# Kernel tuning notes

Hardware: AMD Instinct MI355X
Metric: run time of the kernel (lower is better)

The kernel has to match this reference:

```python
import jax, jax.numpy as jnp
import numpy as np

DT = 0.1
DEATH_THRESHOLD = 0.05


def setup_inputs() -> dict:
    key = jax.random.key(0)
    ks = jax.random.split(key, 12)
    B, S, DE, DM, DC, DEPTH = 1, 4096, 256, 64, 64, 4
    DIN = DE + DC
    w_scale = 0.02  # keeps pre-softmax scores in a sane range
    return {
        "e": jax.random.normal(ks[0], (B, S, DE), jnp.float32),
        "E": jax.random.uniform(ks[1], (B, S, 1), jnp.float32),
        "P": jax.random.uniform(ks[2], (B, S, 1), jnp.float32),
        "G": jax.random.normal(ks[3], (B, S, 1), jnp.float32),
        "m": jax.random.uniform(ks[4], (B, S, DM), jnp.float32),
        "c": jax.random.normal(ks[5], (B, S, DC), jnp.float32),
        "l": jax.random.uniform(ks[6], (B, S, 1), jnp.float32),
        "wq": jax.random.normal(ks[7], (DEPTH, DIN, DE), jnp.float32) * w_scale,
        "bq": jnp.zeros((DEPTH, DE), jnp.float32),
        "wk": jax.random.normal(ks[8], (DEPTH, DIN, DE), jnp.float32) * w_scale,
        "bk": jnp.zeros((DEPTH, DE), jnp.float32),
        "wv": jax.random.normal(ks[9], (DEPTH, DIN, DE), jnp.float32) * w_scale,
        "bv": jnp.zeros((DEPTH, DE), jnp.float32),
        "alpha": jnp.full((DEPTH,), 1.0, jnp.float32),
        "beta": jnp.full((DEPTH,), 0.5, jnp.float32),
        "gamma": jnp.full((DEPTH,), 0.2, jnp.float32),
        "basal": jnp.full((DEPTH,), 0.05, jnp.float32),
    }


def reference(e, E, P, G, m, c, l, wq, bq, wk, bk, wv, bv, alpha, beta, gamma, basal):
    depth = wq.shape[0]
    scale = 1.0 / np.sqrt(wq.shape[-1]).astype(np.float32)
    for i in range(depth):
        # --- OuterTrans: multiplicatively-masked self-attention ---
        x = jnp.concatenate([e, c], axis=-1)                 # [B,S,DE+DC]
        q = x @ wq[i] + bq[i]
        k = x @ wk[i] + bk[i]
        v = x @ wv[i] + bv[i]
        scores = jnp.einsum("bsd,btd->bst", q, k) * scale    # [B,S,S]
        membrane = jnp.einsum("bsd,btd->bst", m, m)          # [B,S,S]
        lifespan = jnp.einsum("bsd,btd->bst", l, l)          # [B,S,S]
        attn = jax.nn.softmax(scores * membrane * lifespan, axis=-1)
        h_tilde = jnp.einsum("bst,btd->bsd", attn, v)        # [B,S,DE]
        e = e + h_tilde
        # --- ThermodynamicODE (elementwise per-token update) ---
        S_in = jnp.sum(h_tilde * h_tilde, axis=-1, keepdims=True)  # ||h||^2 [B,S,1]
        PE = P * E
        P_new = jax.nn.relu(P + (alpha[i] * S_in - beta[i] * PE) * DT)
        E_new = jax.nn.relu(E + (basal[i] - gamma[i] * PE) * DT)
        m_target = jax.nn.sigmoid(E_new - P_new)             # [B,S,1] broadcast to m
        G = G + (0.1 * E_new - 0.5 * P_new) * DT
        l_decay = 0.01 + 0.5 * jax.nn.relu(P_new - 2.0)
        m = 0.9 * m + 0.1 * m_target
        l = jnp.clip(l - l_decay * DT, 0.0, 1.0)
        E, P = E_new, P_new
    # Dynamic pruning: jit-compatible variant -> zero-mask dead cells instead of
    # data-dependent slicing; also return alive_mask and num_died.
    alive = l > DEATH_THRESHOLD                              # [B,S,1] bool
    af = alive.astype(e.dtype)
    num_died = e.shape[1] - jnp.sum(alive.astype(jnp.int32))
    return (e * af, E * af, P * af, G * af, m * af, c * af, l * af,
            alive[0, :, 0], num_died)
```

## Files before the change

### kernel.cpp

```cpp
#include <hip/hip_runtime.h>
#include <hip/hip_bf16.h>
#include <math.h>

#define SS 4096
#define DE 256
#define DM 64
#define DC 64
#define DIN 320
#define DEPTH 4
#define DT_C 0.1f
#define NSPLIT 12
#define BK 32
#define EXP_SHIFT 8.0f

typedef float f32x4_t __attribute__((ext_vector_type(4)));
typedef __bf16 bf16x8_t __attribute__((ext_vector_type(8)));

#define MFMA_BF16(A, B, C) __builtin_amdgcn_mfma_f32_16x16x32_bf16((A), (B), (C), 0, 0, 0)

#define OFF_E     (SS*DE)
#define OFF_P     (OFF_E + SS)
#define OFF_G     (OFF_P + SS)
#define OFF_M     (OFF_G + SS)
#define OFF_C     (OFF_M + SS*DM)
#define OFF_L     (OFF_C + SS*DM)
#define OFF_ALIVE (OFF_L + SS)
#define OFF_DIED  (OFF_ALIVE + SS)

#define WS_EWS   0
#define WS_MWS   (WS_EWS  + SS*DE)
#define WS_EE    (WS_MWS  + SS*DM)
#define WS_PP    (WS_EE   + SS)
#define WS_GG    (WS_PP   + SS)
#define WS_LL    (WS_GG   + SS)
#define WS_PL    (WS_LL   + SS)
#define WS_POB   (WS_PL   + NSPLIT*SS)
#define WS_XB    (WS_POB  + NSPLIT*SS*DE/2)
#define WS_QB    (WS_XB   + SS*DIN/2)
#define WS_KB    (WS_QB   + SS*DE/2)
#define WS_VTB   (WS_KB   + SS*DE/2)
#define WS_MB    (WS_VTB  + SS*DE/2)
#define WS_WT    (WS_MB   + SS*DM/2)
#define WS_SEM   (WS_WT   + 3*DEPTH*DE*DIN/2)

#define KT_STR 264
#define VT_STR 40
#define PJ_STR 72

__global__ __launch_bounds__(256) void transpose_w_kernel(
    const float* __restrict__ wq, const float* __restrict__ wk, const float* __restrict__ wv,
    __hip_bfloat16* __restrict__ wt)
{
    const int zd = blockIdx.z;
    const int z = zd >> 2;
    const float* src = (z == 0 ? wq : (z == 1 ? wk : wv)) + (size_t)(zd & 3) * DIN * DE;
    __shared__ float t[32][33];
    const int k0 = blockIdx.x * 32;
    const int n0 = blockIdx.y * 32;
    const int tr = threadIdx.x >> 5;
    const int tc = threadIdx.x & 31;
    #pragma unroll
    for (int p = 0; p < 4; ++p)
        t[p*8 + tr][tc] = src[(size_t)(k0 + p*8 + tr) * DE + n0 + tc];
    __syncthreads();
    #pragma unroll
    for (int p = 0; p < 4; ++p) {
        int n = n0 + p*8 + tr;
        int k = k0 + tc;
        wt[((size_t)zd * DE + n) * DIN + k] = __float2bfloat16(t[tc][p*8 + tr]);
    }
}

__global__ __launch_bounds__(256) void init_kernel(
    const float* __restrict__ e_in, const float* __restrict__ c_in,
    const float* __restrict__ E_in, const float* __restrict__ P_in,
    const float* __restrict__ G_in, const float* __restrict__ l_in,
    const float* __restrict__ m_in,
    float* __restrict__ e_ws, __hip_bfloat16* __restrict__ xb,
    float* __restrict__ E_ws, float* __restrict__ P_ws, float* __restrict__ G_ws,
    float* __restrict__ l_ws, float* __restrict__ m_ws, __hip_bfloat16* __restrict__ mb,
    int* __restrict__ counters)
{
    const int row = blockIdx.x;
    const int tid = threadIdx.x;
    const float v = e_in[(size_t)row * DE + tid];
    e_ws[(size_t)row * DE + tid] = v;
    xb[(size_t)row * DIN + tid] = __float2bfloat16(v);
    if (tid < DC) {
        xb[(size_t)row * DIN + DE + tid] = __float2bfloat16(c_in[(size_t)row * DC + tid]);
        const float mv = m_in[(size_t)row * DM + tid];
        m_ws[(size_t)row * DM + tid] = mv;
        mb[(size_t)row * DM + tid] = __float2bfloat16(mv);
    }
    if (tid == 0) {
        E_ws[row] = E_in[row];
        P_ws[row] = P_in[row];
        G_ws[row] = G_in[row];
        l_ws[row] = l_in[row];
    }
    if (row == 0 && tid < 2) counters[tid] = 0;
}

__global__ __launch_bounds__(256, 4) void proj_gemm_kernel(
    const __hip_bfloat16* __restrict__ xb, const __hip_bfloat16* __restrict__ wt,
    const float* __restrict__ bq, const float* __restrict__ bk, const float* __restrict__ bv,
    __hip_bfloat16* __restrict__ qb, __hip_bfloat16* __restrict__ kb, __hip_bfloat16* __restrict__ vtb,
    int layer)
{
    __shared__ __align__(16) __hip_bfloat16 at[64 * PJ_STR];
    __shared__ __align__(16) __hip_bfloat16 bt[64 * PJ_STR];
    __shared__ __align__(16) __hip_bfloat16 tt[64 * PJ_STR];

    const int mt = blockIdx.x;
    const int nt4 = blockIdx.y;
    const int row0 = mt * 64;
    const int z = nt4 >> 2;
    const int coln0 = (nt4 & 3) * 64;
    const __hip_bfloat16* wrow = wt + ((size_t)(z * DEPTH + layer) * DE + coln0) * DIN;

    const int tid = threadIdx.x;
    const int w = tid >> 6, lane = tid & 63;
    const int ml = lane & 15, quad = lane >> 4;
    const int s_r = tid >> 2, s_g = tid & 3;

    f32x4_t acc[4];
    #pragma unroll
    for (int nt = 0; nt < 4; ++nt) acc[nt] = (f32x4_t){0.f, 0.f, 0.f, 0.f};

    for (int k0 = 0; k0 < DIN; k0 += 64) {
        __syncthreads();
        {
            const __hip_bfloat16* src = &xb[(size_t)(row0 + s_r) * DIN + k0 + s_g * 16];
            *(float4*)&at[s_r * PJ_STR + s_g * 16]     = *(const float4*)src;
            *(float4*)&at[s_r * PJ_STR + s_g * 16 + 8] = *(const float4*)(src + 8);
        }
        {
            const __hip_bfloat16* src = &wrow[(size_t)s_r * DIN + k0 + s_g * 16];
            *(float4*)&bt[s_r * PJ_STR + s_g * 16]     = *(const float4*)src;
            *(float4*)&bt[s_r * PJ_STR + s_g * 16 + 8] = *(const float4*)(src + 8);
        }
        __syncthreads();
        #pragma unroll
        for (int kk = 0; kk < 2; ++kk) {
            const bf16x8_t a = *(const bf16x8_t*)&at[(w * 16 + ml) * PJ_STR + kk * 32 + quad * 8];
            #pragma unroll
            for (int nt = 0; nt < 4; ++nt) {
                const bf16x8_t b = *(const bf16x8_t*)&bt[(nt * 16 + ml) * PJ_STR + kk * 32 + quad * 8];
                acc[nt] = MFMA_BF16(a, b, acc[nt]);
            }
        }
    }

    const float* bias = (z == 0 ? bq : (z == 1 ? bk : bv)) + (size_t)layer * DE;
    if (z < 2) {
        __hip_bfloat16* O = (z == 0 ? qb : kb);
        #pragma unroll
        for (int nt = 0; nt < 4; ++nt) {
            const int col = coln0 + nt * 16 + ml;
            const float b = bias[col];
            #pragma unroll
            for (int r = 0; r < 4; ++r)
                O[(size_t)(row0 + w * 16 + quad * 4 + r) * DE + col] = __float2bfloat16(acc[nt][r] + b);
        }
    } else {
        #pragma unroll
        for (int nt = 0; nt < 4; ++nt) {
            const int n = nt * 16 + ml;
            const float b = bias[coln0 + n];
            #pragma unroll
            for (int r = 0; r < 4; ++r)
                tt[n * PJ_STR + w * 16 + quad * 4 + r] = __float2bfloat16(acc[nt][r] + b);
        }
        __syncthreads();
        const int c = tid >> 2, seg = tid & 3;
        __hip_bfloat16* dst = &vtb[(size_t)(coln0 + c) * SS + row0 + seg * 16];
        *(float4*)dst       = *(const float4*)&tt[c * PJ_STR + seg * 16];
        *(float4*)(dst + 8) = *(const float4*)&tt[c * PJ_STR + seg * 16 + 8];
    }
}

__global__ __launch_bounds__(256, 3) void attn_mfma_kernel(
    const __hip_bfloat16* __restrict__ qb, const __hip_bfloat16* __restrict__ kb,
    const __hip_bfloat16* __restrict__ vtb, const __hip_bfloat16* __restrict__ mb,
    const float* __restrict__ l_ws,
    __hip_bfloat16* __restrict__ part_ob, float* __restrict__ part_l)
{
    __shared__ __align__(16) __hip_bfloat16 kt[32 * KT_STR];
    __shared__ __align__(16) __hip_bfloat16 vt[256 * VT_STR];

    const int id = blockIdx.x;
    const int split = id >> 6;
    const int rid = id & 63;
    const int qblk = (rid & 7) * 8 + (rid >> 3);

    const int tid = threadIdx.x;
    const int w = tid >> 6, lane = tid & 63;
    const int n = lane & 15, quad = lane >> 4;
    const int row0 = qblk * 64 + w * 16;

    bf16x8_t qa[8];
    #pragma unroll
    for (int kk = 0; kk < 8; ++kk)
        qa[kk] = *(const bf16x8_t*)&qb[(size_t)(row0 + n) * DE + kk * 32 + quad * 8];
    bf16x8_t ma[2];
    #pragma unroll
    for (int kk = 0; kk < 2; ++kk)
        ma[kk] = *(const bf16x8_t*)&mb[(size_t)(row0 + n) * DM + kk * 32 + quad * 8];
    const float lqs = l_ws[row0 + n] * 0.0625f;

    f32x4_t oacc[16];
    #pragma unroll
    for (int ct = 0; ct < 16; ++ct) oacc[ct] = (f32x4_t){0.f, 0.f, 0.f, 0.f};
    float plsum = 0.f;
    const f32x4_t zf4 = (f32x4_t){0.f, 0.f, 0.f, 0.f};

    const int k_row = tid >> 5, k_g = tid & 31;
    const int v_col = tid >> 2, v_seg = tid & 3;
    const int v_base = (v_seg & 1) * 16 + (v_seg >> 1) * 4;

    const int it_begin = (split * 128) / NSPLIT;
    const int it_end   = ((split + 1) * 128) / NSPLIT;

    for (int it = it_begin; it < it_end; ++it) {
        const int t0 = it * BK;
        __syncthreads();
        #pragma unroll
        for (int p = 0; p < 4; ++p) {
            const int row = k_row + p * 8;
            *(float4*)&kt[row * KT_STR + k_g * 8] = *(const float4*)&kb[(size_t)(t0 + row) * DE + k_g * 8];
        }
        #pragma unroll
        for (int p = 0; p < 4; ++p) {
            const int col = v_col + p * 64;
            const float4 f = *(const float4*)&vtb[(size_t)col * SS + t0 + v_seg * 8];
            *(float2*)&vt[col * VT_STR + v_base]     = make_float2(f.x, f.y);
            *(float2*)&vt[col * VT_STR + v_base + 8] = make_float2(f.z, f.w);
        }
        __syncthreads();

        const bf16x8_t mf00 = *(const bf16x8_t*)&mb[(size_t)(t0 + n) * DM + quad * 8];
        const bf16x8_t mf01 = *(const bf16x8_t*)&mb[(size_t)(t0 + n) * DM + 32 + quad * 8];
        const bf16x8_t mf10 = *(const bf16x8_t*)&mb[(size_t)(t0 + n + 16) * DM + quad * 8];
        const bf16x8_t mf11 = *(const bf16x8_t*)&mb[(size_t)(t0 + n + 16) * DM + 32 + quad * 8];
        const float4 lk0 = *(const float4*)&l_ws[t0 + quad * 4];
        const float4 lk1 = *(const float4*)&l_ws[t0 + 16 + quad * 4];

        f32x4_t s0a = zf4, s0b = zf4, s1a = zf4, s1b = zf4;
        #pragma unroll
        for (int kk = 0; kk < 4; ++kk) {
            bf16x8_t k0 = *(const bf16x8_t*)&kt[n * KT_STR + kk * 32 + quad * 8];
            bf16x8_t k1 = *(const bf16x8_t*)&kt[(n + 16) * KT_STR + kk * 32 + quad * 8];
            s0a = MFMA_BF16(k0, qa[kk], s0a);
            s1a = MFMA_BF16(k1, qa[kk], s1a);
        }
        #pragma unroll
        for (int kk = 4; kk < 8; ++kk) {
            bf16x8_t k0 = *(const bf16x8_t*)&kt[n * KT_STR + kk * 32 + quad * 8];
            bf16x8_t k1 = *(const bf16x8_t*)&kt[(n + 16) * KT_STR + kk * 32 + quad * 8];
            s0b = MFMA_BF16(k0, qa[kk], s0b);
            s1b = MFMA_BF16(k1, qa[kk], s1b);
        }
        const f32x4_t st0 = s0a + s0b;
        const f32x4_t st1 = s1a + s1b;

        f32x4_t mm0 = MFMA_BF16(mf00, ma[0], zf4);
        mm0 = MFMA_BF16(mf01, ma[1], mm0);
        f32x4_t mm1 = MFMA_BF16(mf10, ma[0], zf4);
        mm1 = MFMA_BF16(mf11, ma[1], mm1);

        bf16x8_t pa;
        #pragma unroll
        for (int r = 0; r < 4; ++r) {
            const float x0 = st0[r] * lqs * lk0[r] * mm0[r];
            const float x1 = st1[r] * lqs * lk1[r] * mm1[r];
            const float p0 = __expf(x0 - EXP_SHIFT);
            const float p1 = __expf(x1 - EXP_SHIFT);
            plsum += p0 + p1;
            pa[r]     = (__bf16)p0;
            pa[4 + r] = (__bf16)p1;
        }

        #pragma unroll
        for (int ct = 0; ct < 16; ++ct) {
            bf16x8_t vb = *(const bf16x8_t*)&vt[(ct * 16 + n) * VT_STR + quad * 8];
            oacc[ct] = MFMA_BF16(pa, vb, oacc[ct]);
        }
    }

    plsum += __shfl_xor(plsum, 16);
    plsum += __shfl_xor(plsum, 32);
    if (lane < 16)
        part_l[split * SS + row0 + lane] = plsum;

    __hip_bfloat16* dst = part_ob + ((size_t)((split * (SS / 64) + qblk) * 4 + w)) * 4096;
    #pragma unroll
    for (int ct = 0; ct < 16; ++ct) {
        __hip_bfloat16 h4[4];
        #pragma unroll
        for (int r = 0; r < 4; ++r) h4[r] = __float2bfloat16(oacc[ct][r]);
        *(uint2*)&dst[(ct * 64 + lane) * 4] = *(uint2*)h4;
    }
}

__global__ __launch_bounds__(256) void combine_kernel(
    const __hip_bfloat16* __restrict__ part_ob, const float* __restrict__ part_l,
    float* __restrict__ e_ws, __hip_bfloat16* __restrict__ xb,
    float* __restrict__ E_ws, float* __restrict__ P_ws, float* __restrict__ G_ws,
    float* __restrict__ m_ws, __hip_bfloat16* __restrict__ mb, float* __restrict__ l_ws,
    const float* __restrict__ alpha, const float* __restrict__ beta,
    const float* __restrict__ gamma_, const float* __restrict__ basal, int layer)
{
    const int wc = threadIdx.x >> 6, lane = threadIdx.x & 63;
    const int row = blockIdx.x * 4 + wc;
    const int qblk = row >> 6, wa = (row >> 4) & 3, quada = (row >> 2) & 3, ra = row & 3;

    float L = 0.f;
    #pragma unroll
    for (int s = 0; s < NSPLIT; ++s) L += part_l[s * SS + row];
    const float invL = 1.0f / L;

    const int ct = lane >> 2;
    const int base_off = (ct * 64 + quada * 16 + (lane & 3) * 4) * 4;
    float o[4] = {0.f, 0.f, 0.f, 0.f};
    #pragma unroll
    for (int s = 0; s < NSPLIT; ++s) {
        const size_t region = ((size_t)((s * (SS / 64) + qblk) * 4 + wa)) * 4096;
        const ushort* pp = (const ushort*)(part_ob + region) + base_off;
        ushort vals[16];
        *(uint4*)&vals[0] = *(const uint4*)pp;
        *(uint4*)&vals[8] = *(const uint4*)(pp + 8);
        #pragma unroll
        for (int j = 0; j < 4; ++j)
            o[j] += __uint_as_float(((unsigned)vals[j * 4 + ra]) << 16);
    }
    float h0 = o[0] * invL, h1 = o[1] * invL, h2 = o[2] * invL, h3 = o[3] * invL;

    float4 ev = *(float4*)&e_ws[(size_t)row * DE + lane * 4];
    ev.x += h0; ev.y += h1; ev.z += h2; ev.w += h3;
    *(float4*)&e_ws[(size_t)row * DE + lane * 4] = ev;
    {
        __hip_bfloat16 x4[4] = {__float2bfloat16(ev.x), __float2bfloat16(ev.y),
                                __float2bfloat16(ev.z), __float2bfloat16(ev.w)};
        *(uint2*)&xb[(size_t)row * DIN + lane * 4] = *(uint2*)x4;
    }

    float ssq = h0*h0 + h1*h1 + h2*h2 + h3*h3;
    #pragma unroll
    for (int mask = 1; mask < 64; mask <<= 1) ssq += __shfl_xor(ssq, mask);

    const float a = alpha[layer], b = beta[layer], gm = gamma_[layer], bas = basal[layer];
    const float E = E_ws[row], P = P_ws[row];
    const float PE = P * E;
    const float Pn = fmaxf(0.f, P + (a * ssq - b * PE) * DT_C);
    const float En = fmaxf(0.f, E + (bas - gm * PE) * DT_C);
    const float mtg = 1.f / (1.f + __expf(-(En - Pn)));
    const size_t mi = (size_t)row * DM + lane;
    const float mv = 0.9f * m_ws[mi] + 0.1f * mtg;
    m_ws[mi] = mv;
    mb[mi] = __float2bfloat16(mv);
    if (lane == 0) {
        E_ws[row] = En;
        P_ws[row] = Pn;
        G_ws[row] = G_ws[row] + (0.1f * En - 0.5f * Pn) * DT_C;
        const float ldec = 0.01f + 0.5f * fmaxf(0.f, Pn - 2.0f);
        const float lv = l_ws[row] - ldec * DT_C;
        l_ws[row] = fminf(1.f, fmaxf(0.f, lv));
    }
}

__global__ __launch_bounds__(256) void finalizec_kernel(
    const __hip_bfloat16* __restrict__ part_ob, const float* __restrict__ part_l,
    const float* __restrict__ e_ws,
    const float* __restrict__ E_ws, const float* __restrict__ P_ws, const float* __restrict__ G_ws,
    const float* __restrict__ m_ws, const float* __restrict__ c_in, const float* __restrict__ l_ws,
    const float* __restrict__ alpha, const float* __restrict__ beta,
    const float* __restrict__ gamma_, const float* __restrict__ basal,
    float* __restrict__ out, int* __restrict__ counters)
{
    const int rb = blockIdx.x;
    const int tid = threadIdx.x;
    const int wc = tid >> 6, lane = tid & 63;

    const int lp = DEPTH - 1;
    const float a = alpha[lp], bb = beta[lp], gm = gamma_[lp], bas = basal[lp];

    __shared__ int s_alive[4];
    int alive_cnt = 0;

    #pragma unroll
    for (int rr = 0; rr < 4; ++rr) {
        const int row = rb * 16 + wc * 4 + rr;
        const int qb2 = row >> 6, wa = (row >> 4) & 3, quada = (row >> 2) & 3, ra = row & 3;
        float L = 0.f;
        #pragma unroll
        for (int s = 0; s < NSPLIT; ++s) L += part_l[s * SS + row];
        const float invL = 1.0f / L;
        const int ct = lane >> 2;
        const int base_off = (ct * 64 + quada * 16 + (lane & 3) * 4) * 4;
        float o[4] = {0.f, 0.f, 0.f, 0.f};
        #pragma unroll
        for (int s = 0; s < NSPLIT; ++s) {
            const size_t region = ((size_t)((s * (SS / 64) + qb2) * 4 + wa)) * 4096;
            const ushort* pp = (const ushort*)(part_ob + region) + base_off;
            ushort vals[16];
            *(uint4*)&vals[0] = *(const uint4*)pp;
            *(uint4*)&vals[8] = *(const uint4*)(pp + 8);
            #pragma unroll
            for (int j = 0; j < 4; ++j)
                o[j] += __uint_as_float(((unsigned)vals[j * 4 + ra]) << 16);
        }
        const float h0 = o[0] * invL, h1 = o[1] * invL, h2 = o[2] * invL, h3 = o[3] * invL;
        float4 ev = *(const float4*)&e_ws[(size_t)row * DE + lane * 4];
        ev.x += h0; ev.y += h1; ev.z += h2; ev.w += h3;

        float ssq = h0*h0 + h1*h1 + h2*h2 + h3*h3;
        #pragma unroll
        for (int mask = 1; mask < 64; mask <<= 1) ssq += __shfl_xor(ssq, mask);

        const float E = E_ws[row], P = P_ws[row];
        const float PE = P * E;
        const float Pn = fmaxf(0.f, P + (a * ssq - bb * PE) * DT_C);
        const float En = fmaxf(0.f, E + (bas - gm * PE) * DT_C);
        const float mtg = 1.f / (1.f + __expf(-(En - Pn)));
        const float mv = 0.9f * m_ws[(size_t)row * DM + lane] + 0.1f * mtg;
        const float Gn = G_ws[row] + (0.1f * En - 0.5f * Pn) * DT_C;
        const float ldec = 0.01f + 0.5f * fmaxf(0.f, Pn - 2.0f);
        const float lv = fminf(1.f, fmaxf(0.f, l_ws[row] - ldec * DT_C));
        const float af = (lv > 0.05f) ? 1.f : 0.f;

        float4 eo = make_float4(ev.x * af, ev.y * af, ev.z * af, ev.w * af);
        *(float4*)&out[(size_t)row * DE + lane * 4] = eo;
        out[OFF_M + (size_t)row * DM + lane] = mv * af;
        out[OFF_C + (size_t)row * DM + lane] = c_in[(size_t)row * DM + lane] * af;
        if (lane == 0) {
            out[OFF_E + row] = En * af;
            out[OFF_P + row] = Pn * af;
            out[OFF_G + row] = Gn * af;
            out[OFF_L + row] = lv * af;
            out[OFF_ALIVE + row] = af;
            alive_cnt += (af > 0.f) ? 1 : 0;
        }
    }

    if (lane == 0) s_alive[wc] = alive_cnt;
    __syncthreads();
    if (tid == 0) {
        const int blk_alive = s_alive[0] + s_alive[1] + s_alive[2] + s_alive[3];
        atomicAdd(&counters[0], blk_alive);
        __threadfence();
        const int old = atomicAdd(&counters[1], 1);
        if (old == 255) {
            __threadfence();
            const int tot = atomicAdd(&counters[0], 0);
            out[OFF_DIED] = (float)(SS - tot);
        }
    }
}

extern "C" void kernel_launch(void* const* d_in, const int* in_sizes, int n_in,
                              void* d_out, int out_size, void* d_ws, size_t ws_size,
                              hipStream_t stream) {
    const float* e_in = (const float*)d_in[0];
    const float* E_in = (const float*)d_in[1];
    const float* P_in = (const float*)d_in[2];
    const float* G_in = (const float*)d_in[3];
    const float* m_in = (const float*)d_in[4];
    const float* c_in = (const float*)d_in[5];
    const float* l_in = (const float*)d_in[6];
    const float* wq = (const float*)d_in[7];
    const float* bq = (const float*)d_in[8];
    const float* wk = (const float*)d_in[9];
    const float* bk = (const float*)d_in[10];
    const float* wv = (const float*)d_in[11];
    const float* bv = (const float*)d_in[12];
    const float* alpha = (const float*)d_in[13];
    const float* beta  = (const float*)d_in[14];
    const float* gamma_ = (const float*)d_in[15];
    const float* basal = (const float*)d_in[16];
    float* out = (float*)d_out;
    float* ws = (float*)d_ws;

    float* e_ws = ws + WS_EWS;
    float* m_ws = ws + WS_MWS;
    float* E_ws = ws + WS_EE;
    float* P_ws = ws + WS_PP;
    float* G_ws = ws + WS_GG;
    float* l_ws = ws + WS_LL;
    float* part_l = ws + WS_PL;
    __hip_bfloat16* part_ob = (__hip_bfloat16*)(ws + WS_POB);
    __hip_bfloat16* xb  = (__hip_bfloat16*)(ws + WS_XB);
    __hip_bfloat16* qb  = (__hip_bfloat16*)(ws + WS_QB);
    __hip_bfloat16* kb  = (__hip_bfloat16*)(ws + WS_KB);
    __hip_bfloat16* vtb = (__hip_bfloat16*)(ws + WS_VTB);
    __hip_bfloat16* mb  = (__hip_bfloat16*)(ws + WS_MB);
    __hip_bfloat16* wt  = (__hip_bfloat16*)(ws + WS_WT);
    int* counters = (int*)(ws + WS_SEM);

    transpose_w_kernel<<<dim3(DIN/32, DE/32, 12), 256, 0, stream>>>(wq, wk, wv, wt);
    init_kernel<<<dim3(SS), 256, 0, stream>>>(
        e_in, c_in, E_in, P_in, G_in, l_in, m_in,
        e_ws, xb, E_ws, P_ws, G_ws, l_ws, m_ws, mb, counters);

    for (int layer = 0; layer < DEPTH; ++layer) {
        proj_gemm_kernel<<<dim3(SS/64, 12), 256, 0, stream>>>(
            xb, wt, bq, bk, bv, qb, kb, vtb, layer);
        attn_mfma_kernel<<<dim3((SS/64) * NSPLIT), 256, 0, stream>>>(
            qb, kb, vtb, mb, l_ws, part_ob, part_l);
        if (layer < DEPTH - 1)
            combine_kernel<<<dim3(SS/4), 256, 0, stream>>>(
                part_ob, part_l, e_ws, xb, E_ws, P_ws, G_ws, m_ws, mb, l_ws,
                alpha, beta, gamma_, basal, layer);
    }
    finalizec_kernel<<<dim3(SS/16), 256, 0, stream>>>(
        part_ob, part_l, e_ws, E_ws, P_ws, G_ws, m_ws, c_in, l_ws,
        alpha, beta, gamma_, basal, out, counters);
}
```

Baseline: 415.3 us.

## Fuse all layer stages into one persistent cooperative kernel with grid syncs

Replaces the sequence of transpose, init, projection, attention, combine and finalize launches with a single cooperative persistent kernel. Blocks loop over work items of each stage and use grid-wide barriers between stages. This removes per-launch overhead and tail gaps between the roughly fourteen kernels. The cost is grid.sync overhead, occupancy capped by the launch bounds and the shared-memory union, and load imbalance across fixed block counts. The old multi-kernel path stays as a fallback if the cooperative launch fails.

```diff
diff --git a/kernel.cpp b/kernel.cpp
--- a/kernel.cpp
+++ b/kernel.cpp
@@ -1,6 +1,9 @@
 #include <hip/hip_runtime.h>
+#include <hip/hip_cooperative_groups.h>
 #include <hip/hip_bf16.h>
 #include <math.h>
+
+namespace cg = cooperative_groups;
 
 #define SS 4096
 #define DE 256
@@ -12,6 +15,7 @@
 #define NSPLIT 12
 #define BK 32
 #define EXP_SHIFT 8.0f
+#define NBLK_MAX 768
 
 typedef float f32x4_t __attribute__((ext_vector_type(4)));
 typedef __bf16 bf16x8_t __attribute__((ext_vector_type(8)));
@@ -47,6 +51,397 @@
 #define VT_STR 40
 #define PJ_STR 72
 
+struct KParams {
+    const float *e_in, *c_in, *E_in, *P_in, *G_in, *l_in, *m_in;
+    const float *wq, *bq, *wk, *bk, *wv, *bv, *alpha, *beta, *gamma_, *basal;
+    float *e_ws, *m_ws, *E_ws, *P_ws, *G_ws, *l_ws, *part_l;
+    __hip_bfloat16 *part_ob, *xb, *qb, *kb, *vtb, *mb, *wt;
+    int* counters;
+    float* out;
+};
+
+__global__ __launch_bounds__(256, 3) void mega_kernel(KParams p)
+{
+    cg::grid_group grid = cg::this_grid();
+    __shared__ __align__(16) char smem[37376];
+    __shared__ int s_alive[4];
+    const int bid = blockIdx.x;
+    const int tid = threadIdx.x;
+    const int NB = gridDim.x;
+
+    {
+        float (*t)[33] = (float(*)[33])smem;
+        const int tr = tid >> 5, tc = tid & 31;
+        for (int s = bid; s < 960; s += NB) {
+            const int zd = s / 80;
+            const int rem = s % 80;
+            const int k0 = (rem >> 3) * 32;
+            const int n0 = (rem & 7) * 32;
+            const int z = zd >> 2;
+            const float* src = (z == 0 ? p.wq : (z == 1 ? p.wk : p.wv)) + (size_t)(zd & 3) * DIN * DE;
+            __syncthreads();
+            #pragma unroll
+            for (int q = 0; q < 4; ++q)
+                t[q*8 + tr][tc] = src[(size_t)(k0 + q*8 + tr) * DE + n0 + tc];
+            __syncthreads();
+            #pragma unroll
+            for (int q = 0; q < 4; ++q) {
+                const int n = n0 + q*8 + tr;
+                const int k = k0 + tc;
+                p.wt[((size_t)zd * DE + n) * DIN + k] = __float2bfloat16(t[tc][q*8 + tr]);
+            }
+        }
+        for (int row = bid; row < SS; row += NB) {
+            const float v = p.e_in[(size_t)row * DE + tid];
+            p.e_ws[(size_t)row * DE + tid] = v;
+            p.xb[(size_t)row * DIN + tid] = __float2bfloat16(v);
+            if (tid < DC) {
+                p.xb[(size_t)row * DIN + DE + tid] = __float2bfloat16(p.c_in[(size_t)row * DC + tid]);
+                const float mv = p.m_in[(size_t)row * DM + tid];
+                p.m_ws[(size_t)row * DM + tid] = mv;
+                p.mb[(size_t)row * DM + tid] = __float2bfloat16(mv);
+            }
+            if (tid == 0) {
+                p.E_ws[row] = p.E_in[row];
+                p.P_ws[row] = p.P_in[row];
+                p.G_ws[row] = p.G_in[row];
+                p.l_ws[row] = p.l_in[row];
+            }
+        }
+        if (bid == 0 && tid == 0) p.counters[0] = 0;
+    }
+    grid.sync();
+
+    for (int layer = 0; layer < DEPTH; ++layer) {
+        {
+            __hip_bfloat16* at  = (__hip_bfloat16*)smem;
+            __hip_bfloat16* btl = at + 64 * PJ_STR;
+            __hip_bfloat16* tt  = btl + 64 * PJ_STR;
+            const int w = tid >> 6, lane = tid & 63;
+            const int ml = lane & 15, quad = lane >> 4;
+            const int s_r = tid >> 2, s_g = tid & 3;
+
+            for (int s = bid; s < 768; s += NB) {
+                const int mt = s & 63, nt4 = s >> 6;
+                const int row0 = mt * 64;
+                const int z = nt4 >> 2;
+                const int coln0 = (nt4 & 3) * 64;
+                const __hip_bfloat16* wrow = p.wt + ((size_t)(z * DEPTH + layer) * DE + coln0) * DIN;
+
+                f32x4_t acc[4];
+                #pragma unroll
+                for (int nt = 0; nt < 4; ++nt) acc[nt] = (f32x4_t){0.f, 0.f, 0.f, 0.f};
+
+                for (int k0 = 0; k0 < DIN; k0 += 64) {
+                    __syncthreads();
+                    {
+                        const __hip_bfloat16* src = &p.xb[(size_t)(row0 + s_r) * DIN + k0 + s_g * 16];
+                        *(float4*)&at[s_r * PJ_STR + s_g * 16]     = *(const float4*)src;
+                        *(float4*)&at[s_r * PJ_STR + s_g * 16 + 8] = *(const float4*)(src + 8);
+                    }
+                    {
+                        const __hip_bfloat16* src = &wrow[(size_t)s_r * DIN + k0 + s_g * 16];
+                        *(float4*)&btl[s_r * PJ_STR + s_g * 16]     = *(const float4*)src;
+                        *(float4*)&btl[s_r * PJ_STR + s_g * 16 + 8] = *(const float4*)(src + 8);
+                    }
+                    __syncthreads();
+                    #pragma unroll
+                    for (int kk = 0; kk < 2; ++kk) {
+                        const bf16x8_t a = *(const bf16x8_t*)&at[(w * 16 + ml) * PJ_STR + kk * 32 + quad * 8];
+                        #pragma unroll
+                        for (int nt = 0; nt < 4; ++nt) {
+                            const bf16x8_t b = *(const bf16x8_t*)&btl[(nt * 16 + ml) * PJ_STR + kk * 32 + quad * 8];
+                            acc[nt] = MFMA_BF16(a, b, acc[nt]);
+                        }
+                    }
+                }
+
+                const float* bias = (z == 0 ? p.bq : (z == 1 ? p.bk : p.bv)) + (size_t)layer * DE;
+                if (z < 2) {
+                    __hip_bfloat16* O = (z == 0 ? p.qb : p.kb);
+                    #pragma unroll
+                    for (int nt = 0; nt < 4; ++nt) {
+                        const int col = coln0 + nt * 16 + ml;
+                        const float b = bias[col];
+                        #pragma unroll
+                        for (int r = 0; r < 4; ++r)
+                            O[(size_t)(row0 + w * 16 + quad * 4 + r) * DE + col] = __float2bfloat16(acc[nt][r] + b);
+                    }
+                } else {
+                    __syncthreads();
+                    #pragma unroll
+                    for (int nt = 0; nt < 4; ++nt) {
+                        const int n = nt * 16 + ml;
+                        const float b = bias[coln0 + n];
+                        #pragma unroll
+                        for (int r = 0; r < 4; ++r)
+                            tt[n * PJ_STR + w * 16 + quad * 4 + r] = __float2bfloat16(acc[nt][r] + b);
+                    }
+                    __syncthreads();
+                    const int c = tid >> 2, seg = tid & 3;
+                    __hip_bfloat16* dst = &p.vtb[(size_t)(coln0 + c) * SS + row0 + seg * 16];
+                    *(float4*)dst       = *(const float4*)&tt[c * PJ_STR + seg * 16];
+                    *(float4*)(dst + 8) = *(const float4*)&tt[c * PJ_STR + seg * 16 + 8];
+                }
+            }
+        }
+        grid.sync();
+
+        {
+            __hip_bfloat16* kt = (__hip_bfloat16*)smem;
+            __hip_bfloat16* vt = kt + 32 * KT_STR;
+            const int w = tid >> 6, lane = tid & 63;
+            const int n = lane & 15, quad = lane >> 4;
+            const int k_row = tid >> 5, k_g = tid & 31;
+            const int v_col = tid >> 2, v_seg = tid & 3;
+            const int v_base = (v_seg & 1) * 16 + (v_seg >> 1) * 4;
+            const f32x4_t zf4 = (f32x4_t){0.f, 0.f, 0.f, 0.f};
+
+            for (int s = bid; s < 768; s += NB) {
+                const int split = s >> 6;
+                const int rid = s & 63;
+                const int qblk = (rid & 7) * 8 + (rid >> 3);
+                const int row0 = qblk * 64 + w * 16;
+
+                bf16x8_t qa[8];
+                #pragma unroll
+                for (int kk = 0; kk < 8; ++kk)
+                    qa[kk] = *(const bf16x8_t*)&p.qb[(size_t)(row0 + n) * DE + kk * 32 + quad * 8];
+                bf16x8_t ma[2];
+                #pragma unroll
+                for (int kk = 0; kk < 2; ++kk)
+                    ma[kk] = *(const bf16x8_t*)&p.mb[(size_t)(row0 + n) * DM + kk * 32 + quad * 8];
+                const float lqs = p.l_ws[row0 + n] * 0.0625f;
+
+                f32x4_t oacc[16];
+                #pragma unroll
+                for (int ct = 0; ct < 16; ++ct) oacc[ct] = (f32x4_t){0.f, 0.f, 0.f, 0.f};
+                float plsum = 0.f;
+
+                const int it_begin = (split * 128) / NSPLIT;
+                const int it_end   = ((split + 1) * 128) / NSPLIT;
+
+                for (int it = it_begin; it < it_end; ++it) {
+                    const int t0 = it * BK;
+                    __syncthreads();
+                    #pragma unroll
+                    for (int q = 0; q < 4; ++q) {
+                        const int row = k_row + q * 8;
+                        *(float4*)&kt[row * KT_STR + k_g * 8] = *(const float4*)&p.kb[(size_t)(t0 + row) * DE + k_g * 8];
+                    }
+                    #pragma unroll
+                    for (int q = 0; q < 4; ++q) {
+                        const int col = v_col + q * 64;
+                        const float4 f = *(const float4*)&p.vtb[(size_t)col * SS + t0 + v_seg * 8];
+                        *(float2*)&vt[col * VT_STR + v_base]     = make_float2(f.x, f.y);
+                        *(float2*)&vt[col * VT_STR + v_base + 8] = make_float2(f.z, f.w);
+                    }
+                    __syncthreads();
+
+                    const bf16x8_t mf00 = *(const bf16x8_t*)&p.mb[(size_t)(t0 + n) * DM + quad * 8];
+                    const bf16x8_t mf01 = *(const bf16x8_t*)&p.mb[(size_t)(t0 + n) * DM + 32 + quad * 8];
+                    const bf16x8_t mf10 = *(const bf16x8_t*)&p.mb[(size_t)(t0 + n + 16) * DM + quad * 8];
+                    const bf16x8_t mf11 = *(const bf16x8_t*)&p.mb[(size_t)(t0 + n + 16) * DM + 32 + quad * 8];
+                    const float4 lk0 = *(const float4*)&p.l_ws[t0 + quad * 4];
+                    const float4 lk1 = *(const float4*)&p.l_ws[t0 + 16 + quad * 4];
+
+                    f32x4_t s0a = zf4, s0b = zf4, s1a = zf4, s1b = zf4;
+                    #pragma unroll
+                    for (int kk = 0; kk < 4; ++kk) {
+                        bf16x8_t k0 = *(const bf16x8_t*)&kt[n * KT_STR + kk * 32 + quad * 8];
+                        bf16x8_t k1 = *(const bf16x8_t*)&kt[(n + 16) * KT_STR + kk * 32 + quad * 8];
+                        s0a = MFMA_BF16(k0, qa[kk], s0a);
+                        s1a = MFMA_BF16(k1, qa[kk], s1a);
+                    }
+                    #pragma unroll
+                    for (int kk = 4; kk < 8; ++kk) {
+                        bf16x8_t k0 = *(const bf16x8_t*)&kt[n * KT_STR + kk * 32 + quad * 8];
+                        bf16x8_t k1 = *(const bf16x8_t*)&kt[(n + 16) * KT_STR + kk * 32 + quad * 8];
+                        s0b = MFMA_BF16(k0, qa[kk], s0b);
+                        s1b = MFMA_BF16(k1, qa[kk], s1b);
+                    }
+                    const f32x4_t st0 = s0a + s0b;
+                    const f32x4_t st1 = s1a + s1b;
+
+                    f32x4_t mm0 = MFMA_BF16(mf00, ma[0], zf4);
+                    mm0 = MFMA_BF16(mf01, ma[1], mm0);
+                    f32x4_t mm1 = MFMA_BF16(mf10, ma[0], zf4);
+                    mm1 = MFMA_BF16(mf11, ma[1], mm1);
+
+                    bf16x8_t pa;
+                    #pragma unroll
+                    for (int r = 0; r < 4; ++r) {
+                        const float x0 = st0[r] * lqs * lk0[r] * mm0[r];
+                        const float x1 = st1[r] * lqs * lk1[r] * mm1[r];
+                        const float p0 = __expf(x0 - EXP_SHIFT);
+                        const float p1 = __expf(x1 - EXP_SHIFT);
+                        plsum += p0 + p1;
+                        pa[r]     = (__bf16)p0;
+                        pa[4 + r] = (__bf16)p1;
+                    }
+
+                    #pragma unroll
+                    for (int ct = 0; ct < 16; ++ct) {
+                        bf16x8_t vb = *(const bf16x8_t*)&vt[(ct * 16 + n) * VT_STR + quad * 8];
+                        oacc[ct] = MFMA_BF16(pa, vb, oacc[ct]);
+                    }
+                }
+
+                plsum += __shfl_xor(plsum, 16);
+                plsum += __shfl_xor(plsum, 32);
+                if (lane < 16)
+                    p.part_l[split * SS + row0 + lane] = plsum;
+
+                __hip_bfloat16* dst = p.part_ob + ((size_t)((split * (SS / 64) + qblk) * 4 + w)) * 4096;
+                #pragma unroll
+                for (int ct = 0; ct < 16; ++ct) {
+                    __hip_bfloat16 h4[4];
+                    #pragma unroll
+                    for (int r = 0; r < 4; ++r) h4[r] = __float2bfloat16(oacc[ct][r]);
+                    *(uint2*)&dst[(ct * 64 + lane) * 4] = *(uint2*)h4;
+                }
+                __syncthreads();
+            }
+        }
+        grid.sync();
+
+        if (layer < DEPTH - 1) {
+            const int wc = tid >> 6, lane = tid & 63;
+            for (int grp = bid; grp < SS / 4; grp += NB) {
+                const int row = grp * 4 + wc;
+                const int qblk = row >> 6, wa = (row >> 4) & 3, quada = (row >> 2) & 3, ra = row & 3;
+
+                float L = 0.f;
+                #pragma unroll
+                for (int s = 0; s < NSPLIT; ++s) L += p.part_l[s * SS + row];
+                const float invL = 1.0f / L;
+
+                const int ct = lane >> 2;
+                const int base_off = (ct * 64 + quada * 16 + (lane & 3) * 4) * 4;
+                float o[4] = {0.f, 0.f, 0.f, 0.f};
+                #pragma unroll
+                for (int s = 0; s < NSPLIT; ++s) {
+                    const size_t region = ((size_t)((s * (SS / 64) + qblk) * 4 + wa)) * 4096;
+                    const ushort* pp = (const ushort*)(p.part_ob + region) + base_off;
+                    ushort vals[16];
+                    *(uint4*)&vals[0] = *(const uint4*)pp;
+                    *(uint4*)&vals[8] = *(const uint4*)(pp + 8);
+                    #pragma unroll
+                    for (int j = 0; j < 4; ++j)
+                        o[j] += __uint_as_float(((unsigned)vals[j * 4 + ra]) << 16);
+                }
+                const float h0 = o[0] * invL, h1 = o[1] * invL, h2 = o[2] * invL, h3 = o[3] * invL;
+
+                float4 ev = *(float4*)&p.e_ws[(size_t)row * DE + lane * 4];
+                ev.x += h0; ev.y += h1; ev.z += h2; ev.w += h3;
+                *(float4*)&p.e_ws[(size_t)row * DE + lane * 4] = ev;
+                {
+                    __hip_bfloat16 x4[4] = {__float2bfloat16(ev.x), __float2bfloat16(ev.y),
+                                            __float2bfloat16(ev.z), __float2bfloat16(ev.w)};
+                    *(uint2*)&p.xb[(size_t)row * DIN + lane * 4] = *(uint2*)x4;
+                }
+
+                float ssq = h0*h0 + h1*h1 + h2*h2 + h3*h3;
+                #pragma unroll
+                for (int mask = 1; mask < 64; mask <<= 1) ssq += __shfl_xor(ssq, mask);
+
+                const float a = p.alpha[layer], b = p.beta[layer], gm = p.gamma_[layer], bas = p.basal[layer];
+                const float E = p.E_ws[row], P = p.P_ws[row];
+                const float PE = P * E;
+                const float Pn = fmaxf(0.f, P + (a * ssq - b * PE) * DT_C);
+                const float En = fmaxf(0.f, E + (bas - gm * PE) * DT_C);
+                const float mtg = 1.f / (1.f + __expf(-(En - Pn)));
+                const size_t mi = (size_t)row * DM + lane;
+                const float mv = 0.9f * p.m_ws[mi] + 0.1f * mtg;
+                p.m_ws[mi] = mv;
+                p.mb[mi] = __float2bfloat16(mv);
+                if (lane == 0) {
+                    p.E_ws[row] = En;
+                    p.P_ws[row] = Pn;
+                    p.G_ws[row] = p.G_ws[row] + (0.1f * En - 0.5f * Pn) * DT_C;
+                    const float ldec = 0.01f + 0.5f * fmaxf(0.f, Pn - 2.0f);
+                    const float lv = p.l_ws[row] - ldec * DT_C;
+                    p.l_ws[row] = fminf(1.f, fmaxf(0.f, lv));
+                }
+            }
+            grid.sync();
+        }
+    }
+
+    {
+        const int wc = tid >> 6, lane = tid & 63;
+        const int lp = DEPTH - 1;
+        const float a = p.alpha[lp], bb = p.beta[lp], gm = p.gamma_[lp], bas = p.basal[lp];
+
+        for (int grp = bid; grp < SS / 16; grp += NB) {
+            int alive_cnt = 0;
+            #pragma unroll
+            for (int rr = 0; rr < 4; ++rr) {
+                const int row = grp * 16 + wc * 4 + rr;
+                const int qb2 = row >> 6, wa = (row >> 4) & 3, quada = (row >> 2) & 3, ra = row & 3;
+                float L = 0.f;
+                #pragma unroll
+                for (int s = 0; s < NSPLIT; ++s) L += p.part_l[s * SS + row];
+                const float invL = 1.0f / L;
+                const int ct = lane >> 2;
+                const int base_off = (ct * 64 + quada * 16 + (lane & 3) * 4) * 4;
+                float o[4] = {0.f, 0.f, 0.f, 0.f};
+                #pragma unroll
+                for (int s = 0; s < NSPLIT; ++s) {
+                    const size_t region = ((size_t)((s * (SS / 64) + qb2) * 4 + wa)) * 4096;
+                    const ushort* pp = (const ushort*)(p.part_ob + region) + base_off;
+                    ushort vals[16];
+                    *(uint4*)&vals[0] = *(const uint4*)pp;
+                    *(uint4*)&vals[8] = *(const uint4*)(pp + 8);
+                    #pragma unroll
+                    for (int j = 0; j < 4; ++j)
+                        o[j] += __uint_as_float(((unsigned)vals[j * 4 + ra]) << 16);
+                }
+                const float h0 = o[0] * invL, h1 = o[1] * invL, h2 = o[2] * invL, h3 = o[3] * invL;
+                float4 ev = *(const float4*)&p.e_ws[(size_t)row * DE + lane * 4];
+                ev.x += h0; ev.y += h1; ev.z += h2; ev.w += h3;
+
+                float ssq = h0*h0 + h1*h1 + h2*h2 + h3*h3;
+                #pragma unroll
+                for (int mask = 1; mask < 64; mask <<= 1) ssq += __shfl_xor(ssq, mask);
+
+                const float E = p.E_ws[row], P = p.P_ws[row];
+                const float PE = P * E;
+                const float Pn = fmaxf(0.f, P + (a * ssq - bb * PE) * DT_C);
+                const float En = fmaxf(0.f, E + (bas - gm * PE) * DT_C);
+                const float mtg = 1.f / (1.f + __expf(-(En - Pn)));
+                const float mv = 0.9f * p.m_ws[(size_t)row * DM + lane] + 0.1f * mtg;
+                const float Gn = p.G_ws[row] + (0.1f * En - 0.5f * Pn) * DT_C;
+                const float ldec = 0.01f + 0.5f * fmaxf(0.f, Pn - 2.0f);
+                const float lv = fminf(1.f, fmaxf(0.f, p.l_ws[row] - ldec * DT_C));
+                const float af = (lv > 0.05f) ? 1.f : 0.f;
+
+                float4 eo = make_float4(ev.x * af, ev.y * af, ev.z * af, ev.w * af);
+                *(float4*)&p.out[(size_t)row * DE + lane * 4] = eo;
+                p.out[OFF_M + (size_t)row * DM + lane] = mv * af;
+                p.out[OFF_C + (size_t)row * DM + lane] = p.c_in[(size_t)row * DM + lane] * af;
+                if (lane == 0) {
+                    p.out[OFF_E + row] = En * af;
+                    p.out[OFF_P + row] = Pn * af;
+                    p.out[OFF_G + row] = Gn * af;
+                    p.out[OFF_L + row] = lv * af;
+                    p.out[OFF_ALIVE + row] = af;
+                    alive_cnt += (af > 0.f) ? 1 : 0;
+                }
+            }
+            __syncthreads();
+            if (lane == 0) s_alive[wc] = alive_cnt;
+            __syncthreads();
+            if (tid == 0)
+                atomicAdd(&p.counters[0], s_alive[0] + s_alive[1] + s_alive[2] + s_alive[3]);
+            __syncthreads();
+        }
+    }
+    grid.sync();
+    if (bid == 0 && tid == 0)
+        p.out[OFF_DIED] = (float)(SS - p.counters[0]);
+}
+
 __global__ __launch_bounds__(256) void transpose_w_kernel(
     const float* __restrict__ wq, const float* __restrict__ wk, const float* __restrict__ wv,
     __hip_bfloat16* __restrict__ wt)
@@ -60,14 +455,14 @@
     const int tr = threadIdx.x >> 5;
     const int tc = threadIdx.x & 31;
     #pragma unroll
-    for (int p = 0; p < 4; ++p)
-        t[p*8 + tr][tc] = src[(size_t)(k0 + p*8 + tr) * DE + n0 + tc];
+    for (int q = 0; q < 4; ++q)
+        t[q*8 + tr][tc] = src[(size_t)(k0 + q*8 + tr) * DE + n0 + tc];
     __syncthreads();
     #pragma unroll
-    for (int p = 0; p < 4; ++p) {
-        int n = n0 + p*8 + tr;
+    for (int q = 0; q < 4; ++q) {
+        int n = n0 + q*8 + tr;
         int k = k0 + tc;
-        wt[((size_t)zd * DE + n) * DIN + k] = __float2bfloat16(t[tc][p*8 + tr]);
+        wt[((size_t)zd * DE + n) * DIN + k] = __float2bfloat16(t[tc][q*8 + tr]);
     }
 }
 
@@ -225,13 +620,13 @@
         const int t0 = it * BK;
         __syncthreads();
         #pragma unroll
-        for (int p = 0; p < 4; ++p) {
-            const int row = k_row + p * 8;
+        for (int q = 0; q < 4; ++q) {
+            const int row = k_row + q * 8;
             *(float4*)&kt[row * KT_STR + k_g * 8] = *(const float4*)&kb[(size_t)(t0 + row) * DE + k_g * 8];
         }
         #pragma unroll
-        for (int p = 0; p < 4; ++p) {
-            const int col = v_col + p * 64;
+        for (int q = 0; q < 4; ++q) {
+            const int col = v_col + q * 64;
             const float4 f = *(const float4*)&vtb[(size_t)col * SS + t0 + v_seg * 8];
             *(float2*)&vt[col * VT_STR + v_base]     = make_float2(f.x, f.y);
             *(float2*)&vt[col * VT_STR + v_base + 8] = make_float2(f.z, f.w);
@@ -460,58 +855,75 @@
 extern "C" void kernel_launch(void* const* d_in, const int* in_sizes, int n_in,
                               void* d_out, int out_size, void* d_ws, size_t ws_size,
                               hipStream_t stream) {
-    const float* e_in = (const float*)d_in[0];
-    const float* E_in = (const float*)d_in[1];
-    const float* P_in = (const float*)d_in[2];
-    const float* G_in = (const float*)d_in[3];
-    const float* m_in = (const float*)d_in[4];
-    const float* c_in = (const float*)d_in[5];
-    const float* l_in = (const float*)d_in[6];
-    const float* wq = (const float*)d_in[7];
-    const float* bq = (const float*)d_in[8];
-    const float* wk = (const float*)d_in[9];
-    const float* bk = (const float*)d_in[10];
-    const float* wv = (const float*)d_in[11];
-    const float* bv = (const float*)d_in[12];
-    const float* alpha = (const float*)d_in[13];
-    const float* beta  = (const float*)d_in[14];
-    const float* gamma_ = (const float*)d_in[15];
-    const float* basal = (const float*)d_in[16];
-    float* out = (float*)d_out;
     float* ws = (float*)d_ws;
 
-    float* e_ws = ws + WS_EWS;
-    float* m_ws = ws + WS_MWS;
-    float* E_ws = ws + WS_EE;
-    float* P_ws = ws + WS_PP;
-    float* G_ws = ws + WS_GG;
-    float* l_ws = ws + WS_LL;
-    float* part_l = ws + WS_PL;
-    __hip_bfloat16* part_ob = (__hip_bfloat16*)(ws + WS_POB);
-    __hip_bfloat16* xb  = (__hip_bfloat16*)(ws + WS_XB);
-    __hip_bfloat16* qb  = (__hip_bfloat16*)(ws + WS_QB);
-    __hip_bfloat16* kb  = (__hip_bfloat16*)(ws + WS_KB);
-    __hip_bfloat16* vtb = (__hip_bfloat16*)(ws + WS_VTB);
-    __hip_bfloat16* mb  = (__hip_bfloat16*)(ws + WS_MB);
-    __hip_bfloat16* wt  = (__hip_bfloat16*)(ws + WS_WT);
-    int* counters = (int*)(ws + WS_SEM);
-
-    transpose_w_kernel<<<dim3(DIN/32, DE/32, 12), 256, 0, stream>>>(wq, wk, wv, wt);
-    init_kernel<<<dim3(SS), 256, 0, stream>>>(
-        e_in, c_in, E_in, P_in, G_in, l_in, m_in,
-        e_ws, xb, E_ws, P_ws, G_ws, l_ws, m_ws, mb, counters);
-
-    for (int layer = 0; layer < DEPTH; ++layer) {
-        proj_gemm_kernel<<<dim3(SS/64, 12), 256, 0, stream>>>(
-            xb, wt, bq, bk, bv, qb, kb, vtb, layer);
-        attn_mfma_kernel<<<dim3((SS/64) * NSPLIT), 256, 0, stream>>>(
-            qb, kb, vtb, mb, l_ws, part_ob, part_l);
-        if (layer < DEPTH - 1)
-            combine_kernel<<<dim3(SS/4), 256, 0, stream>>>(
-                part_ob, part_l, e_ws, xb, E_ws, P_ws, G_ws, m_ws, mb, l_ws,
-                alpha, beta, gamma_, basal, layer);
-    }
-    finalizec_kernel<<<dim3(SS/16), 256, 0, stream>>>(
-        part_ob, part_l, e_ws, E_ws, P_ws, G_ws, m_ws, c_in, l_ws,
-        alpha, beta, gamma_, basal, out, counters);
+    KParams P;
+    P.e_in  = (const float*)d_in[0];
+    P.E_in  = (const float*)d_in[1];
+    P.P_in  = (const float*)d_in[2];
+    P.G_in  = (const float*)d_in[3];
+    P.m_in  = (const float*)d_in[4];
+    P.c_in  = (const float*)d_in[5];
+    P.l_in  = (const float*)d_in[6];
+    P.wq    = (const float*)d_in[7];
+    P.bq    = (const float*)d_in[8];
+    P.wk    = (const float*)d_in[9];
+    P.bk    = (const float*)d_in[10];
+    P.wv    = (const float*)d_in[11];
+    P.bv    = (const float*)d_in[12];
+    P.alpha = (const float*)d_in[13];
+    P.beta  = (const float*)d_in[14];
+    P.gamma_= (const float*)d_in[15];
+    P.basal = (const float*)d_in[16];
+    P.e_ws  = ws + WS_EWS;
+    P.m_ws  = ws + WS_MWS;
+    P.E_ws  = ws + WS_EE;
+    P.P_ws  = ws + WS_PP;
+    P.G_ws  = ws + WS_GG;
+    P.l_ws  = ws + WS_LL;
+    P.part_l = ws + WS_PL;
+    P.part_ob = (__hip_bfloat16*)(ws + WS_POB);
+    P.xb   = (__hip_bfloat16*)(ws + WS_XB);
+    P.qb   = (__hip_bfloat16*)(ws + WS_QB);
+    P.kb   = (__hip_bfloat16*)(ws + WS_KB);
+    P.vtb  = (__hip_bfloat16*)(ws + WS_VTB);
+    P.mb   = (__hip_bfloat16*)(ws + WS_MB);
+    P.wt   = (__hip_bfloat16*)(ws + WS_WT);
+    P.counters = (int*)(ws + WS_SEM);
+    P.out  = (float*)d_out;
+
+    bool coop_ok = false;
+    int maxPerCU = 0;
+    hipError_t qerr = hipOccupancyMaxActiveBlocksPerMultiprocessor(
+        &maxPerCU, (const void*)mega_kernel, 256, 0);
+    if (qerr == hipSuccess && maxPerCU > 0) {
+        int nblk = maxPerCU * 256;
+        if (nblk > NBLK_MAX) nblk = NBLK_MAX;
+        void* args[] = { (void*)&P };
+        hipError_t lerr = hipLaunchCooperativeKernel(
+            (const void*)mega_kernel, dim3(nblk), dim3(256), args, 0, stream);
+        if (lerr == hipSuccess) coop_ok = true;
+    }
+
+    if (!coop_ok) {
+        transpose_w_kernel<<<dim3(DIN/32, DE/32, 12), 256, 0, stream>>>(
+            P.wq, P.wk, P.wv, P.wt);
+        init_kernel<<<dim3(SS), 256, 0, stream>>>(
+            P.e_in, P.c_in, P.E_in, P.P_in, P.G_in, P.l_in, P.m_in,
+            P.e_ws, P.xb, P.E_ws, P.P_ws, P.G_ws, P.l_ws, P.m_ws, P.mb, P.counters);
+
+        for (int layer = 0; layer < DEPTH; ++layer) {
+            proj_gemm_kernel<<<dim3(SS/64, 12), 256, 0, stream>>>(
+                P.xb, P.wt, P.bq, P.bk, P.bv, P.qb, P.kb, P.vtb, layer);
+            attn_mfma_kernel<<<dim3((SS/64) * NSPLIT), 256, 0, stream>>>(
+                P.qb, P.kb, P.vtb, P.mb, P.l_ws, P.part_ob, P.part_l);
+            if (layer < DEPTH - 1)
+                combine_kernel<<<dim3(SS/4), 256, 0, stream>>>(
+                    P.part_ob, P.part_l, P.e_ws, P.xb, P.E_ws, P.P_ws, P.G_ws,
+                    P.m_ws, P.mb, P.l_ws, P.alpha, P.beta, P.gamma_, P.basal, layer);
+        }
+        finalizec_kernel<<<dim3(SS/16), 256, 0, stream>>>(
+            P.part_ob, P.part_l, P.e_ws, P.E_ws, P.P_ws, P.G_ws, P.m_ws, P.c_in, P.l_ws,
+            P.alpha, P.beta, P.gamma_, P.basal, P.out, P.counters);
+    }
 }
```

After: 1.132 ms. +172.5%, slower.

## Fold weight transpose into init kernel and read K fragments directly from global

Applied to the files above, without the earlier changes.

Merges the bf16 weight-transpose kernel into init_kernel, assigning the first 960 blocks the extra tile-transpose work, which removes one kernel launch. In the attention kernel it drops the LDS staging of K tiles: each lane loads its MFMA K fragments straight from global memory (through cache) instead of cooperatively copying them to shared memory first. This cuts LDS traffic and shared-memory footprint, which may allow higher occupancy, but each wave now re-reads K rows from global/L2 and K loads are no longer coalesced across the block.

```diff
diff --git a/kernel.cpp b/kernel.cpp
--- a/kernel.cpp
+++ b/kernel.cpp
@@ -43,62 +43,60 @@
 #define WS_WT    (WS_MB   + SS*DM/2)
 #define WS_SEM   (WS_WT   + 3*DEPTH*DE*DIN/2)
 
-#define KT_STR 264
 #define VT_STR 40
 #define PJ_STR 72
-
-__global__ __launch_bounds__(256) void transpose_w_kernel(
-    const float* __restrict__ wq, const float* __restrict__ wk, const float* __restrict__ wv,
-    __hip_bfloat16* __restrict__ wt)
-{
-    const int zd = blockIdx.z;
-    const int z = zd >> 2;
-    const float* src = (z == 0 ? wq : (z == 1 ? wk : wv)) + (size_t)(zd & 3) * DIN * DE;
-    __shared__ float t[32][33];
-    const int k0 = blockIdx.x * 32;
-    const int n0 = blockIdx.y * 32;
-    const int tr = threadIdx.x >> 5;
-    const int tc = threadIdx.x & 31;
-    #pragma unroll
-    for (int p = 0; p < 4; ++p)
-        t[p*8 + tr][tc] = src[(size_t)(k0 + p*8 + tr) * DE + n0 + tc];
-    __syncthreads();
-    #pragma unroll
-    for (int p = 0; p < 4; ++p) {
-        int n = n0 + p*8 + tr;
-        int k = k0 + tc;
-        wt[((size_t)zd * DE + n) * DIN + k] = __float2bfloat16(t[tc][p*8 + tr]);
-    }
-}
 
 __global__ __launch_bounds__(256) void init_kernel(
     const float* __restrict__ e_in, const float* __restrict__ c_in,
     const float* __restrict__ E_in, const float* __restrict__ P_in,
     const float* __restrict__ G_in, const float* __restrict__ l_in,
     const float* __restrict__ m_in,
+    const float* __restrict__ wq, const float* __restrict__ wk, const float* __restrict__ wv,
     float* __restrict__ e_ws, __hip_bfloat16* __restrict__ xb,
     float* __restrict__ E_ws, float* __restrict__ P_ws, float* __restrict__ G_ws,
     float* __restrict__ l_ws, float* __restrict__ m_ws, __hip_bfloat16* __restrict__ mb,
-    int* __restrict__ counters)
+    __hip_bfloat16* __restrict__ wt, int* __restrict__ counters)
 {
     const int row = blockIdx.x;
     const int tid = threadIdx.x;
-    const float v = e_in[(size_t)row * DE + tid];
-    e_ws[(size_t)row * DE + tid] = v;
-    xb[(size_t)row * DIN + tid] = __float2bfloat16(v);
-    if (tid < DC) {
-        xb[(size_t)row * DIN + DE + tid] = __float2bfloat16(c_in[(size_t)row * DC + tid]);
-        const float mv = m_in[(size_t)row * DM + tid];
-        m_ws[(size_t)row * DM + tid] = mv;
-        mb[(size_t)row * DM + tid] = __float2bfloat16(mv);
-    }
-    if (tid == 0) {
-        E_ws[row] = E_in[row];
-        P_ws[row] = P_in[row];
-        G_ws[row] = G_in[row];
-        l_ws[row] = l_in[row];
-    }
-    if (row == 0 && tid < 2) counters[tid] = 0;
+    {
+        const float v = e_in[(size_t)row * DE + tid];
+        e_ws[(size_t)row * DE + tid] = v;
+        xb[(size_t)row * DIN + tid] = __float2bfloat16(v);
+        if (tid < DC) {
+            xb[(size_t)row * DIN + DE + tid] = __float2bfloat16(c_in[(size_t)row * DC + tid]);
+            const float mv = m_in[(size_t)row * DM + tid];
+            m_ws[(size_t)row * DM + tid] = mv;
+            mb[(size_t)row * DM + tid] = __float2bfloat16(mv);
+        }
+        if (tid == 0) {
+            E_ws[row] = E_in[row];
+            P_ws[row] = P_in[row];
+            G_ws[row] = G_in[row];
+            l_ws[row] = l_in[row];
+        }
+        if (row == 0 && tid < 2) counters[tid] = 0;
+    }
+    if (row < 960) {
+        __shared__ float t[32][33];
+        const int zd = row / 80;
+        const int rem = row % 80;
+        const int k0 = (rem >> 3) * 32;
+        const int n0 = (rem & 7) * 32;
+        const int z = zd >> 2;
+        const float* src = (z == 0 ? wq : (z == 1 ? wk : wv)) + (size_t)(zd & 3) * DIN * DE;
+        const int tr = tid >> 5, tc = tid & 31;
+        #pragma unroll
+        for (int q = 0; q < 4; ++q)
+            t[q*8 + tr][tc] = src[(size_t)(k0 + q*8 + tr) * DE + n0 + tc];
+        __syncthreads();
+        #pragma unroll
+        for (int q = 0; q < 4; ++q) {
+            const int n = n0 + q*8 + tr;
+            const int k = k0 + tc;
+            wt[((size_t)zd * DE + n) * DIN + k] = __float2bfloat16(t[tc][q*8 + tr]);
+        }
+    }
 }
 
 __global__ __launch_bounds__(256, 4) void proj_gemm_kernel(
@@ -185,7 +183,6 @@
     const float* __restrict__ l_ws,
     __hip_bfloat16* __restrict__ part_ob, float* __restrict__ part_l)
 {
-    __shared__ __align__(16) __hip_bfloat16 kt[32 * KT_STR];
     __shared__ __align__(16) __hip_bfloat16 vt[256 * VT_STR];
 
     const int id = blockIdx.x;
@@ -214,7 +211,6 @@
     float plsum = 0.f;
     const f32x4_t zf4 = (f32x4_t){0.f, 0.f, 0.f, 0.f};
 
-    const int k_row = tid >> 5, k_g = tid & 31;
     const int v_col = tid >> 2, v_seg = tid & 3;
     const int v_base = (v_seg & 1) * 16 + (v_seg >> 1) * 4;
 
@@ -225,18 +221,16 @@
         const int t0 = it * BK;
         __syncthreads();
         #pragma unroll
-        for (int p = 0; p < 4; ++p) {
-            const int row = k_row + p * 8;
-            *(float4*)&kt[row * KT_STR + k_g * 8] = *(const float4*)&kb[(size_t)(t0 + row) * DE + k_g * 8];
-        }
-        #pragma unroll
-        for (int p = 0; p < 4; ++p) {
-            const int col = v_col + p * 64;
+        for (int q = 0; q < 4; ++q) {
+            const int col = v_col + q * 64;
             const float4 f = *(const float4*)&vtb[(size_t)col * SS + t0 + v_seg * 8];
             *(float2*)&vt[col * VT_STR + v_base]     = make_float2(f.x, f.y);
             *(float2*)&vt[col * VT_STR + v_base + 8] = make_float2(f.z, f.w);
         }
         __syncthreads();
+
+        const __hip_bfloat16* krow0 = &kb[(size_t)(t0 + n) * DE + quad * 8];
+        const __hip_bfloat16* krow1 = &kb[(size_t)(t0 + n + 16) * DE + quad * 8];
 
         const bf16x8_t mf00 = *(const bf16x8_t*)&mb[(size_t)(t0 + n) * DM + quad * 8];
         const bf16x8_t mf01 = *(const bf16x8_t*)&mb[(size_t)(t0 + n) * DM + 32 + quad * 8];
@@ -248,15 +242,15 @@
         f32x4_t s0a = zf4, s0b = zf4, s1a = zf4, s1b = zf4;
         #pragma unroll
         for (int kk = 0; kk < 4; ++kk) {
-            bf16x8_t k0 = *(const bf16x8_t*)&kt[n * KT_STR + kk * 32 + quad * 8];
-            bf16x8_t k1 = *(const bf16x8_t*)&kt[(n + 16) * KT_STR + kk * 32 + quad * 8];
+            const bf16x8_t k0 = *(const bf16x8_t*)(krow0 + kk * 32);
+            const bf16x8_t k1 = *(const bf16x8_t*)(krow1 + kk * 32);
             s0a = MFMA_BF16(k0, qa[kk], s0a);
             s1a = MFMA_BF16(k1, qa[kk], s1a);
         }
         #pragma unroll
         for (int kk = 4; kk < 8; ++kk) {
-            bf16x8_t k0 = *(const bf16x8_t*)&kt[n * KT_STR + kk * 32 + quad * 8];
-            bf16x8_t k1 = *(const bf16x8_t*)&kt[(n + 16) * KT_STR + kk * 32 + quad * 8];
+            const bf16x8_t k0 = *(const bf16x8_t*)(krow0 + kk * 32);
+            const bf16x8_t k1 = *(const bf16x8_t*)(krow1 + kk * 32);
             s0b = MFMA_BF16(k0, qa[kk], s0b);
             s1b = MFMA_BF16(k1, qa[kk], s1b);
         }
@@ -496,10 +490,9 @@
     __hip_bfloat16* wt  = (__hip_bfloat16*)(ws + WS_WT);
     int* counters = (int*)(ws + WS_SEM);
 
-    transpose_w_kernel<<<dim3(DIN/32, DE/32, 12), 256, 0, stream>>>(wq, wk, wv, wt);
     init_kernel<<<dim3(SS), 256, 0, stream>>>(
-        e_in, c_in, E_in, P_in, G_in, l_in, m_in,
-        e_ws, xb, E_ws, P_ws, G_ws, l_ws, m_ws, mb, counters);
+        e_in, c_in, E_in, P_in, G_in, l_in, m_in, wq, wk, wv,
+        e_ws, xb, E_ws, P_ws, G_ws, l_ws, m_ws, mb, wt, counters);
 
     for (int layer = 0; layer < DEPTH; ++layer) {
         proj_gemm_kernel<<<dim3(SS/64, 12), 256, 0, stream>>>(
```

Result: slower. 620.7 us (+49.5%).
